# Performance work log

Measured on AMD Instinct MI355X. Metric: run time of the kernel, lower is better.

Reference implementation:

```python
import jax, jax.numpy as jnp
from jax import lax
import numpy as np

# ---- module config (mirrors SSDDecodeLayer init kwargs) ----
IMG_H = 300.0
IMG_W = 300.0
CONF_THRESH = 0.5
IOU_THRESH = 0.45
TOP_K = 200
NMS_MAX = 100          # nms_max_output_size
NUM_CLASSES = 21       # incl. background (class 0, skipped in the loop)
NORMALIZE_COORDS = True
NEG = jnp.float32(-1e30)  # sentinel for suppressed / below-threshold scores


def setup_inputs() -> dict:
    key = jax.random.key(0)
    k1, k2, k3, k4 = jax.random.split(key, 4)
    B, N, C = 64, 8732, NUM_CLASSES
    conf = jax.random.uniform(k1, (B, N, C))                       # class confidences in [0,1]
    loc = jax.random.normal(k2, (B, N, 4)) * 0.1                   # encoded box offsets
    cxcy = jax.random.uniform(k3, (B, N, 2))                       # anchor centers in [0,1]
    wh = jax.random.uniform(k4, (B, N, 2), minval=0.05, maxval=0.3)  # anchor sizes
    var = jnp.broadcast_to(jnp.array([0.1, 0.1, 0.2, 0.2], jnp.float32), (B, N, 4))
    prediction = jnp.concatenate([conf, loc, cxcy, wh, var], axis=-1).astype(jnp.float32)
    return {"prediction": prediction}  # [B, N, NUM_CLASSES + 12]


def _decode(prediction):
    """SSD box decode: offsets * variance * anchor -> corner coords."""
    C = prediction.shape[-1] - 12
    conf = prediction[..., :C]
    loc = prediction[..., C:C + 4]
    anc = prediction[..., C + 4:C + 8]
    var = prediction[..., C + 8:]
    cx = loc[..., 0] * var[..., 0] * anc[..., 2] + anc[..., 0]
    cy = loc[..., 1] * var[..., 1] * anc[..., 3] + anc[..., 1]
    w = jnp.exp(loc[..., 2] * var[..., 2]) * anc[..., 2]
    h = jnp.exp(loc[..., 3] * var[..., 3]) * anc[..., 3]
    xmin = cx - 0.5 * w
    ymin = cy - 0.5 * h
    xmax = cx + 0.5 * w
    ymax = cy + 0.5 * h
    if NORMALIZE_COORDS:
        xmin = xmin * IMG_W
        xmax = xmax * IMG_W
        ymin = ymin * IMG_H
        ymax = ymax * IMG_H
    boxes = jnp.stack([xmin, ymin, xmax, ymax], axis=-1)  # [B, N, 4]
    return conf, boxes


def _iou_one_vs_all(box, boxes):
    """IoU of a single box [4] vs boxes [N,4] (xmin,ymin,xmax,ymax)."""
    ix0 = jnp.maximum(box[0], boxes[:, 0])
    iy0 = jnp.maximum(box[1], boxes[:, 1])
    ix1 = jnp.minimum(box[2], boxes[:, 2])
    iy1 = jnp.minimum(box[3], boxes[:, 3])
    inter = jnp.maximum(ix1 - ix0, 0.0) * jnp.maximum(iy1 - iy0, 0.0)
    a1 = jnp.maximum(box[2] - box[0], 0.0) * jnp.maximum(box[3] - box[1], 0.0)
    a2 = jnp.maximum(boxes[:, 2] - boxes[:, 0], 0.0) * jnp.maximum(boxes[:, 3] - boxes[:, 1], 0.0)
    return inter / jnp.maximum(a1 + a2 - inter, 1e-8)


def _greedy_nms(boxes, scores):
    """Fixed-shape greedy NMS: returns (indices [NMS_MAX], valid [NMS_MAX]).
    Matches tf.image.non_max_suppression semantics (suppress IoU > threshold)
    after the score > CONF_THRESH boolean mask."""
    s0 = jnp.where(scores > CONF_THRESH, scores, NEG)

    def step(s, _):
        best = jnp.argmax(s)
        ok = s[best] > NEG * 0.5      # still a real (unsuppressed, above-thresh) box
        iou = _iou_one_vs_all(boxes[best], boxes)
        s = jnp.where(iou > IOU_THRESH, NEG, s)  # suppresses best itself (IoU=1)
        return s, (best, ok)

    _, (idx, ok) = lax.scan(step, s0, None, length=NMS_MAX)
    return idx, ok


def _per_image(conf, boxes):
    """conf [N, C], boxes [N, 4] -> [TOP_K, 6] rows of (class_id, score, xmin, ymin, xmax, ymax)."""
    dtype = conf.dtype
    cls_ids = jnp.arange(1, conf.shape[-1], dtype=dtype)  # skip background class 0
    cls_scores = conf[:, 1:].T                            # [C-1, N]

    def per_class(cid, scores):
        idx, ok = _greedy_nms(boxes, scores)
        okf = ok.astype(dtype)[:, None]
        rows = jnp.concatenate(
            [jnp.full((NMS_MAX, 1), cid, dtype=dtype),
             scores[idx][:, None],
             boxes[idx]], axis=-1) * okf                  # zero-pad invalid slots
        return rows                                       # [NMS_MAX, 6]

    rows = jax.vmap(per_class)(cls_ids, cls_scores)       # [C-1, NMS_MAX, 6]
    flat = rows.reshape(-1, 6)                            # [(C-1)*NMS_MAX, 6]
    _, tk_idx = lax.top_k(flat[:, 1], TOP_K)              # top-k by confidence
    return flat[tk_idx]                                   # [TOP_K, 6]


def reference(prediction):
    conf, boxes = _decode(prediction)
    return jax.vmap(_per_image)(conf, boxes)              # [B, TOP_K, 6]
```

## Files before the change

kernel.cpp:

```cpp
#include <hip/hip_runtime.h>
#include <math.h>


#pragma clang fp contract(off)

#define NANCH 8732
#define NB 64
#define NCLS 20
#define NMSMAX 100
#define TOPK 200
#define PRED_STRIDE 33
#define NTHR 512
#define NE 18
#define NBUCK 2048
#define NEGF -1e30f
#define DTILE 64

__device__ __forceinline__ unsigned flipf(float f) {
  unsigned u = __float_as_uint(f);
  return u ^ ((u >> 31) ? 0xFFFFFFFFu : 0x80000000u);
}

__device__ __forceinline__ float unflipf(unsigned se) {
  unsigned sbits = (se & 0x80000000u) ? (se ^ 0x80000000u) : ~se;
  return __uint_as_float(sbits);
}

__device__ __forceinline__ int bucket_of(float s) {
  float t = (s - 0.5f) * 4096.0f;
  int b = (int)t;
  b = b < 0 ? 0 : (b > (NBUCK - 1) ? (NBUCK - 1) : b);
  return (NBUCK - 1) - b;
}

__device__ __forceinline__ bool iou_gt(float inter, float den) {
  const double THR = (double)0.45f + 0x1.0p-26;
  return (double)inter > THR * (double)den;
}

__device__ __forceinline__ float rdlanef(float v, int l) {
  return __uint_as_float(__builtin_amdgcn_readlane(__float_as_uint(v), l));
}

__global__ __launch_bounds__(256) void decode_kernel(
    const float* __restrict__ pred,
    float* __restrict__ boxes,
    float* __restrict__ scores_t) {
#pragma clang fp contract(off)
  const int b = blockIdx.y;
  const int n0 = blockIdx.x * DTILE;
  const int na = (NANCH - n0) < DTILE ? (NANCH - n0) : DTILE;
  const int tid = threadIdx.x;
  const int l = tid & 63;

  __shared__ float lds[DTILE * PRED_STRIDE];

  const float* src = pred + ((long long)b * NANCH + n0) * PRED_STRIDE;
  const int tot = na * PRED_STRIDE;
  for (int e = tid; e < tot; e += 256) lds[e] = src[e];
  __syncthreads();

  if (tid < 64 && l < na) {
    const float* row = lds + l * PRED_STRIDE;
    float l0 = row[21], l1 = row[22], l2 = row[23], l3 = row[24];
    float ax = row[25], ay = row[26], aw = row[27], ah = row[28];
    float v0 = row[29], v1 = row[30], v2 = row[31], v3 = row[32];

    float cx = (l0 * v0) * aw + ax;
    float cy = (l1 * v1) * ah + ay;
    float e2 = (float)exp((double)(l2 * v2));
    float e3 = (float)exp((double)(l3 * v3));
    float w = e2 * aw;
    float h = e3 * ah;
    float hw = 0.5f * w, hh = 0.5f * h;
    float xmin = (cx - hw) * 300.0f;
    float ymin = (cy - hh) * 300.0f;
    float xmax = (cx + hw) * 300.0f;
    float ymax = (cy + hh) * 300.0f;
    *(float4*)(boxes + ((long long)b * NANCH + n0 + l) * 4) =
        make_float4(xmin, ymin, xmax, ymax);
  }

  if (scores_t) {
#pragma unroll
    for (int it = 0; it < 5; ++it) {
      int c = (tid >> 6) + (it << 2);
      if (l < na) {
        scores_t[((long long)b * NCLS + c) * NANCH + n0 + l] =
            lds[l * PRED_STRIDE + 1 + c];
      }
    }
  }
}

__global__ __launch_bounds__(NTHR) void sort_kernel(
    const float* __restrict__ scores_t,
    unsigned short* __restrict__ sidx,
    int* __restrict__ ncand_g) {
#pragma clang fp contract(off)
  const int g = blockIdx.x;
  const int b = g / NCLS;
  const int c1 = g % NCLS;
  const int tid = threadIdx.x;
  const int lane = tid & 63;
  const int wid = tid >> 6;

  __shared__ unsigned long long keys[NANCH];
  __shared__ unsigned off[NBUCK];
  __shared__ unsigned wsum[8];

  const float* srow = scores_t + ((long long)b * NCLS + c1) * NANCH;

  for (int q = 0; q < NBUCK / NTHR; ++q) off[tid + q * NTHR] = 0u;
  __syncthreads();

  unsigned sflip[NE];
  short bkt[NE];
#pragma unroll
  for (int k = 0; k < NE; ++k) {
    int i = tid + (k << 9);
    bkt[k] = -1;
    if (i < NANCH) {
      float s = srow[i];
      if (s > 0.5f) {
        int bb = bucket_of(s);
        bkt[k] = (short)bb;
        sflip[k] = flipf(s);
        atomicAdd(&off[bb], 1u);
      }
    }
  }
  __syncthreads();

  {
    unsigned v0 = off[(tid << 2) + 0], v1 = off[(tid << 2) + 1];
    unsigned v2 = off[(tid << 2) + 2], v3 = off[(tid << 2) + 3];
    unsigned ls = v0 + v1 + v2 + v3;
    unsigned x = ls;
#pragma unroll
    for (int d = 1; d < 64; d <<= 1) {
      unsigned y = __shfl_up(x, d);
      if (lane >= d) x += y;
    }
    if (lane == 63) wsum[wid] = x;
    __syncthreads();
    unsigned wbase = 0;
    for (int w = 0; w < wid; ++w) wbase += wsum[w];
    unsigned base = wbase + x - ls;
    off[(tid << 2) + 0] = base;
    off[(tid << 2) + 1] = base + v0;
    off[(tid << 2) + 2] = base + v0 + v1;
    off[(tid << 2) + 3] = base + v0 + v1 + v2;
  }
  __syncthreads();

#pragma unroll
  for (int k = 0; k < NE; ++k) {
    if (bkt[k] >= 0) {
      int i = tid + (k << 9);
      unsigned long long key = ((unsigned long long)sflip[k] << 32) |
                               (unsigned)(0xFFFFFFFFu - (unsigned)i);
      unsigned slot = atomicAdd(&off[(int)bkt[k]], 1u);
      keys[slot] = key;
    }
  }
  __syncthreads();

  for (int q = 0; q < NBUCK / NTHR; ++q) {
    int bk = tid * (NBUCK / NTHR) + q;
    int st = bk ? (int)off[bk - 1] : 0;
    int en = (int)off[bk];
    for (int i = st + 1; i < en; ++i) {
      unsigned long long k = keys[i];
      int j = i - 1;
      while (j >= st && keys[j] < k) { keys[j + 1] = keys[j]; --j; }
      keys[j + 1] = k;
    }
  }
  __syncthreads();

  const int ncand = (int)off[NBUCK - 1];

  unsigned short* sg = sidx + (long long)g * NANCH;
  for (int s = tid; s < ncand; s += NTHR) {
    sg[s] = (unsigned short)(0xFFFFFFFFu - (unsigned)(keys[s] & 0xFFFFFFFFu));
  }
  if (tid == 0) ncand_g[g] = ncand;
}

__global__ __launch_bounds__(64) void scan_kernel(
    const float* __restrict__ boxes,
    const float* __restrict__ scores_t,
    const unsigned short* __restrict__ sidx,
    const int* __restrict__ ncand_g,
    float* __restrict__ rows) {
#pragma clang fp contract(off)
  const int g = blockIdx.x;
  const int b = g / NCLS;
  const int c1 = g % NCLS;
  const int lane = threadIdx.x;

  __shared__ float4 accb[NMSMAX];
  __shared__ float acca[NMSMAX];

  const float* bimg = boxes + (long long)b * NANCH * 4;
  const float* srow = scores_t + ((long long)b * NCLS + c1) * NANCH;
  const unsigned short* sg = sidx + (long long)g * NANCH;
  float* grow = rows + (long long)g * NMSMAX * 6;

  const int ncand = ncand_g[g];
  int nacc = 0;

  if (ncand > 0) {
    const float fcls = (float)(c1 + 1);
    const int nchunk = (ncand + 63) >> 6;

    int cl0 = lane < ncand ? lane : ncand - 1;
    unsigned id0 = sg[cl0];
    float4 cbv = *(const float4*)(bimg + (long long)id0 * 4);
    float scv = srow[id0];

    for (int c = 0; c < nchunk && nacc < NMSMAX; ++c) {
      float4 cbn = make_float4(0.f, 0.f, 0.f, 0.f);
      float scn = 0.f;
      if (c + 1 < nchunk) {
        int sl = ((c + 1) << 6) + lane;
        int cl = sl < ncand ? sl : ncand - 1;
        unsigned id = sg[cl];
        cbn = *(const float4*)(bimg + (long long)id * 4);
        scn = srow[id];
      }

      const float4 cb = cbv;
      const float sc = scv;
      const float ca = fmaxf(cb.z - cb.x, 0.f) * fmaxf(cb.w - cb.y, 0.f);
      bool su = ((c << 6) + lane) >= ncand;

      for (int j = 0; j < nacc; ++j) {
        float4 ab = accb[j];
        float aa = acca[j];
        float ix0 = fmaxf(ab.x, cb.x), iy0 = fmaxf(ab.y, cb.y);
        float ix1 = fminf(ab.z, cb.z), iy1 = fminf(ab.w, cb.w);
        float inter = fmaxf(ix1 - ix0, 0.f) * fmaxf(iy1 - iy0, 0.f);
        float den = fmaxf((aa + ca) - inter, 1e-8f);
        su = su || iou_gt(inter, den);
      }

      unsigned long long live = __ballot(!su);
      while (live && nacc < NMSMAX) {
        int l = __ffsll(live) - 1;
        float bx = rdlanef(cb.x, l), by = rdlanef(cb.y, l);
        float bz = rdlanef(cb.z, l), bw = rdlanef(cb.w, l);
        float bs = rdlanef(sc, l);
        float aa = fmaxf(bz - bx, 0.f) * fmaxf(bw - by, 0.f);
        if (lane == 0) {
          float* gr = grow + nacc * 6;
          gr[0] = fcls;
          gr[1] = bs;
          gr[2] = bx; gr[3] = by; gr[4] = bz; gr[5] = bw;
          accb[nacc] = make_float4(bx, by, bz, bw);
          acca[nacc] = aa;
        }
        ++nacc;
        float ix0 = fmaxf(bx, cb.x), iy0 = fmaxf(by, cb.y);
        float ix1 = fminf(bz, cb.z), iy1 = fminf(bw, cb.w);
        float inter = fmaxf(ix1 - ix0, 0.f) * fmaxf(iy1 - iy0, 0.f);
        float den = fmaxf((aa + ca) - inter, 1e-8f);
        su = su || iou_gt(inter, den) || (lane == l);
        live = __ballot(!su);
      }

      cbv = cbn; scv = scn;
    }
  }

  for (int j = nacc * 6 + lane; j < NMSMAX * 6; j += 64) grow[j] = 0.f;
}

__global__ __launch_bounds__(NTHR) void nms_fused_kernel(
    const float* __restrict__ boxes,
    const float* __restrict__ scores_t,
    const float* __restrict__ pred,
    float* __restrict__ rows) {
#pragma clang fp contract(off)
  const int g = blockIdx.x;
  const int b = g / NCLS;
  const int c1 = g % NCLS;
  const int tid = threadIdx.x;
  const int lane = tid & 63;
  const int wid = tid >> 6;

  __shared__ unsigned long long keys[NANCH];
  __shared__ unsigned off[NBUCK];
  __shared__ unsigned wsum[8];
  __shared__ float4 accb[NMSMAX];
  __shared__ float acca[NMSMAX];
  __shared__ int nacc_s;

  const float* bimg = boxes + (long long)b * NANCH * 4;
  float* grow = rows + (long long)g * NMSMAX * 6;

  for (int q = 0; q < NBUCK / NTHR; ++q) off[tid + q * NTHR] = 0u;
  __syncthreads();

  unsigned sflip[NE];
  short bkt[NE];
#pragma unroll
  for (int k = 0; k < NE; ++k) {
    int i = tid + (k << 9);
    bkt[k] = -1;
    if (i < NANCH) {
      float s = scores_t
          ? scores_t[((long long)b * NCLS + c1) * NANCH + i]
          : pred[((long long)b * NANCH + i) * PRED_STRIDE + 1 + c1];
      if (s > 0.5f) {
        int bb = bucket_of(s);
        bkt[k] = (short)bb;
        sflip[k] = flipf(s);
        atomicAdd(&off[bb], 1u);
      }
    }
  }
  __syncthreads();

  {
    unsigned v0 = off[(tid << 2) + 0], v1 = off[(tid << 2) + 1];
    unsigned v2 = off[(tid << 2) + 2], v3 = off[(tid << 2) + 3];
    unsigned ls = v0 + v1 + v2 + v3;
    unsigned x = ls;
#pragma unroll
    for (int d = 1; d < 64; d <<= 1) {
      unsigned y = __shfl_up(x, d);
      if (lane >= d) x += y;
    }
    if (lane == 63) wsum[wid] = x;
    __syncthreads();
    unsigned wbase = 0;
    for (int w = 0; w < wid; ++w) wbase += wsum[w];
    unsigned base = wbase + x - ls;
    off[(tid << 2) + 0] = base;
    off[(tid << 2) + 1] = base + v0;
    off[(tid << 2) + 2] = base + v0 + v1;
    off[(tid << 2) + 3] = base + v0 + v1 + v2;
  }
  __syncthreads();

#pragma unroll
  for (int k = 0; k < NE; ++k) {
    if (bkt[k] >= 0) {
      int i = tid + (k << 9);
      unsigned long long key = ((unsigned long long)sflip[k] << 32) |
                               (unsigned)(0xFFFFFFFFu - (unsigned)i);
      unsigned slot = atomicAdd(&off[(int)bkt[k]], 1u);
      keys[slot] = key;
    }
  }
  __syncthreads();

  for (int q = 0; q < NBUCK / NTHR; ++q) {
    int bk = tid * (NBUCK / NTHR) + q;
    int st = bk ? (int)off[bk - 1] : 0;
    int en = (int)off[bk];
    for (int i = st + 1; i < en; ++i) {
      unsigned long long k = keys[i];
      int j = i - 1;
      while (j >= st && keys[j] < k) { keys[j + 1] = keys[j]; --j; }
      keys[j + 1] = k;
    }
  }
  __syncthreads();

  const int ncand = (int)off[NBUCK - 1];

  if (wid == 0 && ncand > 0) {
    const float fcls = (float)(c1 + 1);
    int nacc = 0;
    const int nchunk = (ncand + 63) >> 6;

    int slot0 = lane < ncand ? lane : 0;
    unsigned long long kcur = keys[slot0];
    float4 cbv;
    {
      unsigned bidx = 0xFFFFFFFFu - (unsigned)(kcur & 0xFFFFFFFFu);
      cbv = *(const float4*)(bimg + (long long)bidx * 4);
    }

    for (int c = 0; c < nchunk && nacc < NMSMAX; ++c) {
      unsigned long long knxt = 0ull;
      float4 cbn = make_float4(0.f, 0.f, 0.f, 0.f);
      if (c + 1 < nchunk) {
        int sl = ((c + 1) << 6) + lane;
        int cl = sl < ncand ? sl : 0;
        knxt = keys[cl];
        unsigned bidx = 0xFFFFFFFFu - (unsigned)(knxt & 0xFFFFFFFFu);
        cbn = *(const float4*)(bimg + (long long)bidx * 4);
      }

      const float4 cb = cbv;
      const float ca = fmaxf(cb.z - cb.x, 0.f) * fmaxf(cb.w - cb.y, 0.f);
      bool su = ((c << 6) + lane) >= ncand;

      for (int j = 0; j < nacc; ++j) {
        float4 ab = accb[j];
        float aa = acca[j];
        float ix0 = fmaxf(ab.x, cb.x), iy0 = fmaxf(ab.y, cb.y);
        float ix1 = fminf(ab.z, cb.z), iy1 = fminf(ab.w, cb.w);
        float inter = fmaxf(ix1 - ix0, 0.f) * fmaxf(iy1 - iy0, 0.f);
        float den = fmaxf((aa + ca) - inter, 1e-8f);
        su = su || iou_gt(inter, den);
      }

      unsigned long long live = __ballot(!su);
      while (live && nacc < NMSMAX) {
        int l = __ffsll(live) - 1;
        float bx = rdlanef(cb.x, l), by = rdlanef(cb.y, l);
        float bz = rdlanef(cb.z, l), bw = rdlanef(cb.w, l);
        unsigned khi = __builtin_amdgcn_readlane((unsigned)(kcur >> 32), l);
        float aa = fmaxf(bz - bx, 0.f) * fmaxf(bw - by, 0.f);
        if (lane == 0) {
          float* gr = grow + nacc * 6;
          gr[0] = fcls;
          gr[1] = unflipf(khi);
          gr[2] = bx; gr[3] = by; gr[4] = bz; gr[5] = bw;
          accb[nacc] = make_float4(bx, by, bz, bw);
          acca[nacc] = aa;
        }
        ++nacc;
        float ix0 = fmaxf(bx, cb.x), iy0 = fmaxf(by, cb.y);
        float ix1 = fminf(bz, cb.z), iy1 = fminf(bw, cb.w);
        float inter = fmaxf(ix1 - ix0, 0.f) * fmaxf(iy1 - iy0, 0.f);
        float den = fmaxf((aa + ca) - inter, 1e-8f);
        su = su || iou_gt(inter, den) || (lane == l);
        live = __ballot(!su);
      }

      kcur = knxt; cbv = cbn;
    }
    if (lane == 0) nacc_s = nacc;
  } else if (tid == 0 && ncand == 0) {
    nacc_s = 0;
  }
  __syncthreads();

  for (int j = nacc_s * 6 + tid; j < NMSMAX * 6; j += NTHR) grow[j] = 0.f;
}

__global__ __launch_bounds__(512) void topk_kernel(const float* __restrict__ rows,
                                                   float* __restrict__ out) {
  __shared__ unsigned long long key[2048];
  const int b = blockIdx.x;
  const int tid = threadIdx.x;
  const float* rb = rows + (long long)b * (NCLS * NMSMAX) * 6;

  for (int e = tid; e < 2048; e += 512) {
    unsigned long long k = 0ull;
    if (e < NCLS * NMSMAX) {
      float s = rb[e * 6 + 1];
      unsigned se = flipf(s);
      k = ((unsigned long long)se << 32) | (unsigned)(0xFFFFFFFFu - (unsigned)e);
    }
    key[e] = k;
  }
  __syncthreads();

  for (unsigned k2 = 2; k2 <= 2048; k2 <<= 1) {
    for (unsigned j = k2 >> 1; j > 0; j >>= 1) {
      for (unsigned t = tid; t < 1024; t += 512) {
        unsigned i = t + (t & ~(j - 1));
        unsigned l = i + j;
        bool up = ((i & k2) == 0);
        unsigned long long a = key[i], c = key[l];
        if (up ? (a < c) : (a > c)) { key[i] = c; key[l] = a; }
      }
      __syncthreads();
    }
  }

  if (tid < TOPK) {
    unsigned long long kk = key[tid];
    unsigned e = 0xFFFFFFFFu - (unsigned)(kk & 0xFFFFFFFFu);
    const float* src = rb + (long long)e * 6;
    float* dst = out + ((long long)b * TOPK + tid) * 6;
#pragma unroll
    for (int j = 0; j < 6; ++j) dst[j] = src[j];
  }
}

extern "C" void kernel_launch(void* const* d_in, const int* in_sizes, int n_in,
                              void* d_out, int out_size, void* d_ws, size_t ws_size,
                              hipStream_t stream) {
  const float* pred = (const float*)d_in[0];
  float* out = (float*)d_out;
  float* ws = (float*)d_ws;

  const long long boxes_f = (long long)NB * NANCH * 4;
  const long long rows_f  = (long long)NB * NCLS * NMSMAX * 6;
  const long long st_f    = (long long)NB * NCLS * NANCH;
  const long long sidx_f  = (long long)NB * NCLS * NANCH / 2;
  const long long ncand_f = NB * NCLS;

  float* boxes = ws;
  float* rows  = ws + boxes_f;
  float* st    = ws + boxes_f + rows_f;
  unsigned short* sidx = (unsigned short*)(ws + boxes_f + rows_f + st_f);
  int* ncand = (int*)(ws + boxes_f + rows_f + st_f + sidx_f);

  size_t need_scores = (size_t)(boxes_f + rows_f + st_f) * sizeof(float);
  size_t need_full   = (size_t)(boxes_f + rows_f + st_f + sidx_f + ncand_f) * sizeof(float);

  bool have_scores = ws_size >= need_scores;
  bool full = ws_size >= need_full;
  float* scores_t = have_scores ? st : nullptr;

  dim3 dgrid((NANCH + DTILE - 1) / DTILE, NB);
  decode_kernel<<<dgrid, 256, 0, stream>>>(pred, boxes, scores_t);

  if (full) {
    sort_kernel<<<NB * NCLS, NTHR, 0, stream>>>(scores_t, sidx, ncand);
    scan_kernel<<<NB * NCLS, 64, 0, stream>>>(boxes, scores_t, sidx, ncand, rows);
  } else {
    nms_fused_kernel<<<NB * NCLS, NTHR, 0, stream>>>(boxes, scores_t, pred, rows);
  }
  topk_kernel<<<NB, 512, 0, stream>>>(rows, out);
}
```

Before: 240.3 us.

## Replace per-bucket insertion sort with 64-wide warp bitonic chunk sort in NMS sort

The sort kernel now scatters 16-bit anchor indices into LDS instead of 64-bit keys, and reads scores with float4 loads. When no bucket holds more than 64 candidates, it groups consecutive buckets into chunks of at most 64 and sorts each chunk with a wave-level bitonic shuffle sort, spreading chunks across the 8 waves. Otherwise it falls back to an insertion sort that re-reads scores from global memory. The decode kernel now processes 256 anchors per block with one thread per anchor writing all 20 class scores. The fused fallback kernel gets the same fast path. The gain depends on the bucket-occupancy check holding for typical inputs, and the added chunking loop and global score reloads add overhead.

```diff
diff --git a/kernel.cpp b/kernel.cpp
--- a/kernel.cpp
+++ b/kernel.cpp
@@ -5,6 +5,7 @@
 #pragma clang fp contract(off)
 
 #define NANCH 8732
+#define NF4 2183
 #define NB 64
 #define NCLS 20
 #define NMSMAX 100
@@ -13,8 +14,7 @@
 #define NTHR 512
 #define NE 18
 #define NBUCK 2048
-#define NEGF -1e30f
-#define DTILE 64
+#define DTILE 256
 
 __device__ __forceinline__ unsigned flipf(float f) {
   unsigned u = __float_as_uint(f);
@@ -51,7 +51,6 @@
   const int n0 = blockIdx.x * DTILE;
   const int na = (NANCH - n0) < DTILE ? (NANCH - n0) : DTILE;
   const int tid = threadIdx.x;
-  const int l = tid & 63;
 
   __shared__ float lds[DTILE * PRED_STRIDE];
 
@@ -60,8 +59,8 @@
   for (int e = tid; e < tot; e += 256) lds[e] = src[e];
   __syncthreads();
 
-  if (tid < 64 && l < na) {
-    const float* row = lds + l * PRED_STRIDE;
+  if (tid < na) {
+    const float* row = lds + tid * PRED_STRIDE;
     float l0 = row[21], l1 = row[22], l2 = row[23], l3 = row[24];
     float ax = row[25], ay = row[26], aw = row[27], ah = row[28];
     float v0 = row[29], v1 = row[30], v2 = row[31], v3 = row[32];
@@ -77,17 +76,14 @@
     float ymin = (cy - hh) * 300.0f;
     float xmax = (cx + hw) * 300.0f;
     float ymax = (cy + hh) * 300.0f;
-    *(float4*)(boxes + ((long long)b * NANCH + n0 + l) * 4) =
+    *(float4*)(boxes + ((long long)b * NANCH + n0 + tid) * 4) =
         make_float4(xmin, ymin, xmax, ymax);
-  }
-
-  if (scores_t) {
-#pragma unroll
-    for (int it = 0; it < 5; ++it) {
-      int c = (tid >> 6) + (it << 2);
-      if (l < na) {
-        scores_t[((long long)b * NCLS + c) * NANCH + n0 + l] =
-            lds[l * PRED_STRIDE + 1 + c];
+
+    if (scores_t) {
+#pragma unroll
+      for (int c = 0; c < NCLS; ++c) {
+        scores_t[((long long)b * NCLS + c) * NANCH + n0 + tid] =
+            lds[tid * PRED_STRIDE + 1 + c];
       }
     }
   }
@@ -105,29 +101,33 @@
   const int lane = tid & 63;
   const int wid = tid >> 6;
 
-  __shared__ unsigned long long keys[NANCH];
+  __shared__ unsigned short sidx_s[NANCH];
   __shared__ unsigned off[NBUCK];
   __shared__ unsigned wsum[8];
+  __shared__ int maxb_s;
 
   const float* srow = scores_t + ((long long)b * NCLS + c1) * NANCH;
 
   for (int q = 0; q < NBUCK / NTHR; ++q) off[tid + q * NTHR] = 0u;
-  __syncthreads();
-
-  unsigned sflip[NE];
-  short bkt[NE];
-#pragma unroll
-  for (int k = 0; k < NE; ++k) {
-    int i = tid + (k << 9);
-    bkt[k] = -1;
-    if (i < NANCH) {
-      float s = srow[i];
-      if (s > 0.5f) {
-        int bb = bucket_of(s);
-        bkt[k] = (short)bb;
-        sflip[k] = flipf(s);
-        atomicAdd(&off[bb], 1u);
-      }
+  if (tid == 0) maxb_s = 0;
+  __syncthreads();
+
+  short bkt[20];
+#pragma unroll
+  for (int it = 0; it < 5; ++it) {
+    int f4 = tid + it * NTHR;
+    bool valid = f4 < NF4;
+    float4 sv = valid ? ((const float4*)srow)[f4]
+                      : make_float4(0.f, 0.f, 0.f, 0.f);
+    float ss[4] = {sv.x, sv.y, sv.z, sv.w};
+#pragma unroll
+    for (int c = 0; c < 4; ++c) {
+      short bb = -1;
+      if (valid && ss[c] > 0.5f) {
+        bb = (short)bucket_of(ss[c]);
+        atomicAdd(&off[(int)bb], 1u);
+      }
+      bkt[it * 4 + c] = bb;
     }
   }
   __syncthreads();
@@ -135,6 +135,10 @@
   {
     unsigned v0 = off[(tid << 2) + 0], v1 = off[(tid << 2) + 1];
     unsigned v2 = off[(tid << 2) + 2], v3 = off[(tid << 2) + 3];
+    unsigned mv = v0 > v1 ? v0 : v1;
+    unsigned mv2 = v2 > v3 ? v2 : v3;
+    mv = mv > mv2 ? mv : mv2;
+    if (mv > 64u) atomicMax(&maxb_s, (int)mv);
     unsigned ls = v0 + v1 + v2 + v3;
     unsigned x = ls;
 #pragma unroll
@@ -155,36 +159,89 @@
   __syncthreads();
 
 #pragma unroll
-  for (int k = 0; k < NE; ++k) {
-    if (bkt[k] >= 0) {
-      int i = tid + (k << 9);
-      unsigned long long key = ((unsigned long long)sflip[k] << 32) |
-                               (unsigned)(0xFFFFFFFFu - (unsigned)i);
-      unsigned slot = atomicAdd(&off[(int)bkt[k]], 1u);
-      keys[slot] = key;
-    }
-  }
-  __syncthreads();
-
-  for (int q = 0; q < NBUCK / NTHR; ++q) {
-    int bk = tid * (NBUCK / NTHR) + q;
-    int st = bk ? (int)off[bk - 1] : 0;
-    int en = (int)off[bk];
-    for (int i = st + 1; i < en; ++i) {
-      unsigned long long k = keys[i];
-      int j = i - 1;
-      while (j >= st && keys[j] < k) { keys[j + 1] = keys[j]; --j; }
-      keys[j + 1] = k;
+  for (int it = 0; it < 5; ++it) {
+#pragma unroll
+    for (int c = 0; c < 4; ++c) {
+      short bb = bkt[it * 4 + c];
+      if (bb >= 0) {
+        int i = (tid + it * NTHR) * 4 + c;
+        unsigned slot = atomicAdd(&off[(int)bb], 1u);
+        sidx_s[slot] = (unsigned short)i;
+      }
     }
   }
   __syncthreads();
 
   const int ncand = (int)off[NBUCK - 1];
-
   unsigned short* sg = sidx + (long long)g * NANCH;
-  for (int s = tid; s < ncand; s += NTHR) {
-    sg[s] = (unsigned short)(0xFFFFFFFFu - (unsigned)(keys[s] & 0xFFFFFFFFu));
-  }
+
+  if (maxb_s == 0) {
+    int s0 = 0, bcur = 0, cidx = 0;
+    while (s0 < ncand) {
+      int bend = bcur;
+      while (true) {
+        int bi = bend + lane;
+        bool ok = (bi < NBUCK) && ((off[bi] - (unsigned)s0) <= 64u);
+        unsigned long long bal = __ballot(ok);
+        int cnt = __popcll(bal);
+        if (cnt == 64 && bend + 64 < NBUCK) { bend += 64; continue; }
+        bend += cnt;
+        break;
+      }
+      int send = (int)off[bend - 1];
+      int csz = send - s0;
+      bcur = bend;
+      if (csz > 0) {
+        if ((cidx & 7) == wid) {
+          unsigned long long v = 0ull;
+          if (lane < csz) {
+            unsigned id = sidx_s[s0 + lane];
+            float s = srow[id];
+            v = ((unsigned long long)flipf(s) << 32) |
+                (unsigned)(0xFFFFFFFFu - id);
+          }
+#pragma unroll
+          for (int k = 2; k <= 64; k <<= 1) {
+#pragma unroll
+            for (int j = k >> 1; j >= 1; j >>= 1) {
+              unsigned long long o = __shfl_xor(v, j);
+              bool keep_max = (((lane & k) == 0) == ((lane & j) == 0));
+              v = keep_max ? (v >= o ? v : o) : (v >= o ? o : v);
+            }
+          }
+          if (lane < csz) {
+            sg[s0 + lane] =
+                (unsigned short)(0xFFFFFFFFu - (unsigned)(v & 0xFFFFFFFFu));
+          }
+        }
+        ++cidx;
+      }
+      s0 = send;
+    }
+  } else {
+    for (int q = 0; q < NBUCK / NTHR; ++q) {
+      int bk = tid * (NBUCK / NTHR) + q;
+      int st = bk ? (int)off[bk - 1] : 0;
+      int en = (int)off[bk];
+      for (int i = st + 1; i < en; ++i) {
+        unsigned short id = sidx_s[i];
+        float s = srow[id];
+        int j = i - 1;
+        while (j >= st) {
+          unsigned short jd = sidx_s[j];
+          float js = srow[jd];
+          bool jless = (js < s) || (js == s && jd > id);
+          if (!jless) break;
+          sidx_s[j + 1] = jd;
+          --j;
+        }
+        sidx_s[j + 1] = id;
+      }
+    }
+    __syncthreads();
+    for (int s = tid; s < ncand; s += NTHR) sg[s] = sidx_s[s];
+  }
+
   if (tid == 0) ncand_g[g] = ncand;
 }
 
@@ -277,9 +334,49 @@
   for (int j = nacc * 6 + lane; j < NMSMAX * 6; j += 64) grow[j] = 0.f;
 }
 
+__global__ __launch_bounds__(512) void topk_kernel(const float* __restrict__ rows,
+                                                   float* __restrict__ out) {
+  __shared__ unsigned long long key[2048];
+  const int b = blockIdx.x;
+  const int tid = threadIdx.x;
+  const float* rb = rows + (long long)b * (NCLS * NMSMAX) * 6;
+
+  for (int e = tid; e < 2048; e += 512) {
+    unsigned long long k = 0ull;
+    if (e < NCLS * NMSMAX) {
+      float s = rb[e * 6 + 1];
+      unsigned se = flipf(s);
+      k = ((unsigned long long)se << 32) | (unsigned)(0xFFFFFFFFu - (unsigned)e);
+    }
+    key[e] = k;
+  }
+  __syncthreads();
+
+  for (unsigned k2 = 2; k2 <= 2048; k2 <<= 1) {
+    for (unsigned j = k2 >> 1; j > 0; j >>= 1) {
+      for (unsigned t = tid; t < 1024; t += 512) {
+        unsigned i = t + (t & ~(j - 1));
+        unsigned l = i + j;
+        bool up = ((i & k2) == 0);
+        unsigned long long a = key[i], c = key[l];
+        if (up ? (a < c) : (a > c)) { key[i] = c; key[l] = a; }
+      }
+      __syncthreads();
+    }
+  }
+
+  if (tid < TOPK) {
+    unsigned long long kk = key[tid];
+    unsigned e = 0xFFFFFFFFu - (unsigned)(kk & 0xFFFFFFFFu);
+    const float* src = rb + (long long)e * 6;
+    float* dst = out + ((long long)b * TOPK + tid) * 6;
+#pragma unroll
+    for (int j = 0; j < 6; ++j) dst[j] = src[j];
+  }
+}
+
 __global__ __launch_bounds__(NTHR) void nms_fused_kernel(
     const float* __restrict__ boxes,
-    const float* __restrict__ scores_t,
     const float* __restrict__ pred,
     float* __restrict__ rows) {
 #pragma clang fp contract(off)
@@ -296,11 +393,13 @@
   __shared__ float4 accb[NMSMAX];
   __shared__ float acca[NMSMAX];
   __shared__ int nacc_s;
+  __shared__ int maxb_s;
 
   const float* bimg = boxes + (long long)b * NANCH * 4;
   float* grow = rows + (long long)g * NMSMAX * 6;
 
   for (int q = 0; q < NBUCK / NTHR; ++q) off[tid + q * NTHR] = 0u;
+  if (tid == 0) maxb_s = 0;
   __syncthreads();
 
   unsigned sflip[NE];
@@ -310,9 +409,7 @@
     int i = tid + (k << 9);
     bkt[k] = -1;
     if (i < NANCH) {
-      float s = scores_t
-          ? scores_t[((long long)b * NCLS + c1) * NANCH + i]
-          : pred[((long long)b * NANCH + i) * PRED_STRIDE + 1 + c1];
+      float s = pred[((long long)b * NANCH + i) * PRED_STRIDE + 1 + c1];
       if (s > 0.5f) {
         int bb = bucket_of(s);
         bkt[k] = (short)bb;
@@ -326,6 +423,10 @@
   {
     unsigned v0 = off[(tid << 2) + 0], v1 = off[(tid << 2) + 1];
     unsigned v2 = off[(tid << 2) + 2], v3 = off[(tid << 2) + 3];
+    unsigned mv = v0 > v1 ? v0 : v1;
+    unsigned mv2 = v2 > v3 ? v2 : v3;
+    mv = mv > mv2 ? mv : mv2;
+    if (mv > 64u) atomicMax(&maxb_s, (int)mv);
     unsigned ls = v0 + v1 + v2 + v3;
     unsigned x = ls;
 #pragma unroll
@@ -357,133 +458,170 @@
   }
   __syncthreads();
 
-  for (int q = 0; q < NBUCK / NTHR; ++q) {
-    int bk = tid * (NBUCK / NTHR) + q;
-    int st = bk ? (int)off[bk - 1] : 0;
-    int en = (int)off[bk];
-    for (int i = st + 1; i < en; ++i) {
-      unsigned long long k = keys[i];
-      int j = i - 1;
-      while (j >= st && keys[j] < k) { keys[j + 1] = keys[j]; --j; }
-      keys[j + 1] = k;
-    }
-  }
-  __syncthreads();
-
   const int ncand = (int)off[NBUCK - 1];
-
-  if (wid == 0 && ncand > 0) {
+  const bool fastp = (maxb_s == 0);
+
+  if (!fastp) {
+    for (int q = 0; q < NBUCK / NTHR; ++q) {
+      int bk = tid * (NBUCK / NTHR) + q;
+      int st = bk ? (int)off[bk - 1] : 0;
+      int en = (int)off[bk];
+      for (int i = st + 1; i < en; ++i) {
+        unsigned long long k = keys[i];
+        int j = i - 1;
+        while (j >= st && keys[j] < k) { keys[j + 1] = keys[j]; --j; }
+        keys[j + 1] = k;
+      }
+    }
+    __syncthreads();
+  }
+
+  if (wid == 0) {
     const float fcls = (float)(c1 + 1);
     int nacc = 0;
-    const int nchunk = (ncand + 63) >> 6;
-
-    int slot0 = lane < ncand ? lane : 0;
-    unsigned long long kcur = keys[slot0];
-    float4 cbv;
-    {
-      unsigned bidx = 0xFFFFFFFFu - (unsigned)(kcur & 0xFFFFFFFFu);
-      cbv = *(const float4*)(bimg + (long long)bidx * 4);
-    }
-
-    for (int c = 0; c < nchunk && nacc < NMSMAX; ++c) {
-      unsigned long long knxt = 0ull;
-      float4 cbn = make_float4(0.f, 0.f, 0.f, 0.f);
-      if (c + 1 < nchunk) {
-        int sl = ((c + 1) << 6) + lane;
-        int cl = sl < ncand ? sl : 0;
-        knxt = keys[cl];
-        unsigned bidx = 0xFFFFFFFFu - (unsigned)(knxt & 0xFFFFFFFFu);
-        cbn = *(const float4*)(bimg + (long long)bidx * 4);
-      }
-
-      const float4 cb = cbv;
-      const float ca = fmaxf(cb.z - cb.x, 0.f) * fmaxf(cb.w - cb.y, 0.f);
-      bool su = ((c << 6) + lane) >= ncand;
-
-      for (int j = 0; j < nacc; ++j) {
-        float4 ab = accb[j];
-        float aa = acca[j];
-        float ix0 = fmaxf(ab.x, cb.x), iy0 = fmaxf(ab.y, cb.y);
-        float ix1 = fminf(ab.z, cb.z), iy1 = fminf(ab.w, cb.w);
-        float inter = fmaxf(ix1 - ix0, 0.f) * fmaxf(iy1 - iy0, 0.f);
-        float den = fmaxf((aa + ca) - inter, 1e-8f);
-        su = su || iou_gt(inter, den);
-      }
-
-      unsigned long long live = __ballot(!su);
-      while (live && nacc < NMSMAX) {
-        int l = __ffsll(live) - 1;
-        float bx = rdlanef(cb.x, l), by = rdlanef(cb.y, l);
-        float bz = rdlanef(cb.z, l), bw = rdlanef(cb.w, l);
-        unsigned khi = __builtin_amdgcn_readlane((unsigned)(kcur >> 32), l);
-        float aa = fmaxf(bz - bx, 0.f) * fmaxf(bw - by, 0.f);
-        if (lane == 0) {
-          float* gr = grow + nacc * 6;
-          gr[0] = fcls;
-          gr[1] = unflipf(khi);
-          gr[2] = bx; gr[3] = by; gr[4] = bz; gr[5] = bw;
-          accb[nacc] = make_float4(bx, by, bz, bw);
-          acca[nacc] = aa;
-        }
-        ++nacc;
-        float ix0 = fmaxf(bx, cb.x), iy0 = fmaxf(by, cb.y);
-        float ix1 = fminf(bz, cb.z), iy1 = fminf(bw, cb.w);
-        float inter = fmaxf(ix1 - ix0, 0.f) * fmaxf(iy1 - iy0, 0.f);
-        float den = fmaxf((aa + ca) - inter, 1e-8f);
-        su = su || iou_gt(inter, den) || (lane == l);
-        live = __ballot(!su);
-      }
-
-      kcur = knxt; cbv = cbn;
-    }
+
+    if (ncand > 0 && fastp) {
+      int s0 = 0, bcur = 0;
+      while (s0 < ncand && nacc < NMSMAX) {
+        int bend = bcur;
+        while (true) {
+          int bi = bend + lane;
+          bool ok = false;
+          if (bi < NBUCK) ok = (off[bi] - (unsigned)s0) <= 64u;
+          unsigned long long bal = __ballot(ok);
+          int cnt = __popcll(bal);
+          if (cnt == 64 && bend + 64 < NBUCK) { bend += 64; continue; }
+          bend += cnt;
+          break;
+        }
+        int send = (int)off[bend - 1];
+        int csz = send - s0;
+        bcur = bend;
+        if (csz == 0) { s0 = send; continue; }
+
+        unsigned long long v = (lane < csz) ? keys[s0 + lane] : 0ull;
+#pragma unroll
+        for (int k = 2; k <= 64; k <<= 1) {
+#pragma unroll
+          for (int j = k >> 1; j >= 1; j >>= 1) {
+            unsigned long long o = __shfl_xor(v, j);
+            bool keep_max = (((lane & k) == 0) == ((lane & j) == 0));
+            v = keep_max ? (v >= o ? v : o) : (v >= o ? o : v);
+          }
+        }
+
+        float4 cb = make_float4(0.f, 0.f, 0.f, 0.f);
+        if (lane < csz) {
+          unsigned bidx = 0xFFFFFFFFu - (unsigned)(v & 0xFFFFFFFFu);
+          cb = *(const float4*)(bimg + (long long)bidx * 4);
+        }
+        const float ca = fmaxf(cb.z - cb.x, 0.f) * fmaxf(cb.w - cb.y, 0.f);
+        bool su = lane >= csz;
+
+        for (int j = 0; j < nacc; ++j) {
+          float4 ab = accb[j];
+          float aa = acca[j];
+          float ix0 = fmaxf(ab.x, cb.x), iy0 = fmaxf(ab.y, cb.y);
+          float ix1 = fminf(ab.z, cb.z), iy1 = fminf(ab.w, cb.w);
+          float inter = fmaxf(ix1 - ix0, 0.f) * fmaxf(iy1 - iy0, 0.f);
+          float den = fmaxf((aa + ca) - inter, 1e-8f);
+          su = su || iou_gt(inter, den);
+        }
+
+        unsigned long long live = __ballot(!su);
+        while (live && nacc < NMSMAX) {
+          int l = __ffsll(live) - 1;
+          float bx = rdlanef(cb.x, l), by = rdlanef(cb.y, l);
+          float bz = rdlanef(cb.z, l), bw = rdlanef(cb.w, l);
+          unsigned khi = __builtin_amdgcn_readlane((unsigned)(v >> 32), l);
+          float aa = fmaxf(bz - bx, 0.f) * fmaxf(bw - by, 0.f);
+          if (lane == 0) {
+            float* gr = grow + nacc * 6;
+            gr[0] = fcls;
+            gr[1] = unflipf(khi);
+            gr[2] = bx; gr[3] = by; gr[4] = bz; gr[5] = bw;
+            accb[nacc] = make_float4(bx, by, bz, bw);
+            acca[nacc] = aa;
+          }
+          ++nacc;
+          float ix0 = fmaxf(bx, cb.x), iy0 = fmaxf(by, cb.y);
+          float ix1 = fminf(bz, cb.z), iy1 = fminf(bw, cb.w);
+          float inter = fmaxf(ix1 - ix0, 0.f) * fmaxf(iy1 - iy0, 0.f);
+          float den = fmaxf((aa + ca) - inter, 1e-8f);
+          su = su || iou_gt(inter, den) || (lane == l);
+          live = __ballot(!su);
+        }
+
+        s0 = send;
+      }
+    } else if (ncand > 0) {
+      const int nchunk = (ncand + 63) >> 6;
+      int slot0 = lane < ncand ? lane : 0;
+      unsigned long long kcur = keys[slot0];
+      float4 cbv;
+      {
+        unsigned bidx = 0xFFFFFFFFu - (unsigned)(kcur & 0xFFFFFFFFu);
+        cbv = *(const float4*)(bimg + (long long)bidx * 4);
+      }
+
+      for (int c = 0; c < nchunk && nacc < NMSMAX; ++c) {
+        unsigned long long knxt = 0ull;
+        float4 cbn = make_float4(0.f, 0.f, 0.f, 0.f);
+        if (c + 1 < nchunk) {
+          int sl = ((c + 1) << 6) + lane;
+          int cl = sl < ncand ? sl : 0;
+          knxt = keys[cl];
+          unsigned bidx = 0xFFFFFFFFu - (unsigned)(knxt & 0xFFFFFFFFu);
+          cbn = *(const float4*)(bimg + (long long)bidx * 4);
+        }
+
+        const float4 cb = cbv;
+        const float ca = fmaxf(cb.z - cb.x, 0.f) * fmaxf(cb.w - cb.y, 0.f);
+        bool su = ((c << 6) + lane) >= ncand;
+
+        for (int j = 0; j < nacc; ++j) {
+          float4 ab = accb[j];
+          float aa = acca[j];
+          float ix0 = fmaxf(ab.x, cb.x), iy0 = fmaxf(ab.y, cb.y);
+          float ix1 = fminf(ab.z, cb.z), iy1 = fminf(ab.w, cb.w);
+          float inter = fmaxf(ix1 - ix0, 0.f) * fmaxf(iy1 - iy0, 0.f);
+          float den = fmaxf((aa + ca) - inter, 1e-8f);
+          su = su || iou_gt(inter, den);
+        }
+
+        unsigned long long live = __ballot(!su);
+        while (live && nacc < NMSMAX) {
+          int l = __ffsll(live) - 1;
+          float bx = rdlanef(cb.x, l), by = rdlanef(cb.y, l);
+          float bz = rdlanef(cb.z, l), bw = rdlanef(cb.w, l);
+          unsigned khi = __builtin_amdgcn_readlane((unsigned)(kcur >> 32), l);
+          float aa = fmaxf(bz - bx, 0.f) * fmaxf(bw - by, 0.f);
+          if (lane == 0) {
+            float* gr = grow + nacc * 6;
+            gr[0] = fcls;
+            gr[1] = unflipf(khi);
+            gr[2] = bx; gr[3] = by; gr[4] = bz; gr[5] = bw;
+            accb[nacc] = make_float4(bx, by, bz, bw);
+            acca[nacc] = aa;
+          }
+          ++nacc;
+          float ix0 = fmaxf(bx, cb.x), iy0 = fmaxf(by, cb.y);
+          float ix1 = fminf(bz, cb.z), iy1 = fminf(bw, cb.w);
+          float inter = fmaxf(ix1 - ix0, 0.f) * fmaxf(iy1 - iy0, 0.f);
+          float den = fmaxf((aa + ca) - inter, 1e-8f);
+          su = su || iou_gt(inter, den) || (lane == l);
+          live = __ballot(!su);
+        }
+
+        kcur = knxt; cbv = cbn;
+      }
+    }
+
     if (lane == 0) nacc_s = nacc;
-  } else if (tid == 0 && ncand == 0) {
-    nacc_s = 0;
   }
   __syncthreads();
 
   for (int j = nacc_s * 6 + tid; j < NMSMAX * 6; j += NTHR) grow[j] = 0.f;
-}
-
-__global__ __launch_bounds__(512) void topk_kernel(const float* __restrict__ rows,
-                                                   float* __restrict__ out) {
-  __shared__ unsigned long long key[2048];
-  const int b = blockIdx.x;
-  const int tid = threadIdx.x;
-  const float* rb = rows + (long long)b * (NCLS * NMSMAX) * 6;
-
-  for (int e = tid; e < 2048; e += 512) {
-    unsigned long long k = 0ull;
-    if (e < NCLS * NMSMAX) {
-      float s = rb[e * 6 + 1];
-      unsigned se = flipf(s);
-      k = ((unsigned long long)se << 32) | (unsigned)(0xFFFFFFFFu - (unsigned)e);
-    }
-    key[e] = k;
-  }
-  __syncthreads();
-
-  for (unsigned k2 = 2; k2 <= 2048; k2 <<= 1) {
-    for (unsigned j = k2 >> 1; j > 0; j >>= 1) {
-      for (unsigned t = tid; t < 1024; t += 512) {
-        unsigned i = t + (t & ~(j - 1));
-        unsigned l = i + j;
-        bool up = ((i & k2) == 0);
-        unsigned long long a = key[i], c = key[l];
-        if (up ? (a < c) : (a > c)) { key[i] = c; key[l] = a; }
-      }
-      __syncthreads();
-    }
-  }
-
-  if (tid < TOPK) {
-    unsigned long long kk = key[tid];
-    unsigned e = 0xFFFFFFFFu - (unsigned)(kk & 0xFFFFFFFFu);
-    const float* src = rb + (long long)e * 6;
-    float* dst = out + ((long long)b * TOPK + tid) * 6;
-#pragma unroll
-    for (int j = 0; j < 6; ++j) dst[j] = src[j];
-  }
 }
 
 extern "C" void kernel_launch(void* const* d_in, const int* in_sizes, int n_in,
@@ -505,21 +643,18 @@
   unsigned short* sidx = (unsigned short*)(ws + boxes_f + rows_f + st_f);
   int* ncand = (int*)(ws + boxes_f + rows_f + st_f + sidx_f);
 
-  size_t need_scores = (size_t)(boxes_f + rows_f + st_f) * sizeof(float);
-  size_t need_full   = (size_t)(boxes_f + rows_f + st_f + sidx_f + ncand_f) * sizeof(float);
-
-  bool have_scores = ws_size >= need_scores;
+  size_t need_full = (size_t)(boxes_f + rows_f + st_f + sidx_f + ncand_f) * sizeof(float);
   bool full = ws_size >= need_full;
-  float* scores_t = have_scores ? st : nullptr;
 
   dim3 dgrid((NANCH + DTILE - 1) / DTILE, NB);
-  decode_kernel<<<dgrid, 256, 0, stream>>>(pred, boxes, scores_t);
 
   if (full) {
-    sort_kernel<<<NB * NCLS, NTHR, 0, stream>>>(scores_t, sidx, ncand);
-    scan_kernel<<<NB * NCLS, 64, 0, stream>>>(boxes, scores_t, sidx, ncand, rows);
+    decode_kernel<<<dgrid, 256, 0, stream>>>(pred, boxes, st);
+    sort_kernel<<<NB * NCLS, NTHR, 0, stream>>>(st, sidx, ncand);
+    scan_kernel<<<NB * NCLS, 64, 0, stream>>>(boxes, st, sidx, ncand, rows);
   } else {
-    nms_fused_kernel<<<NB * NCLS, NTHR, 0, stream>>>(boxes, scores_t, pred, rows);
+    decode_kernel<<<dgrid, 256, 0, stream>>>(pred, boxes, nullptr);
+    nms_fused_kernel<<<NB * NCLS, NTHR, 0, stream>>>(boxes, pred, rows);
   }
   topk_kernel<<<NB, 512, 0, stream>>>(rows, out);
 }
```

New measurement: 259.7 us. 8.0% more time.
